# Performance work log

Hardware: AMD Instinct MI355X
Metric: run time of the kernel (lower is better)

Reference implementation:

```python
import jax, jax.numpy as jnp
import numpy as np

NUM_HEADS = 8
FREQ_RATIO = 0.5

def setup_inputs() -> dict:
    key = jax.random.key(0)
    ks = jax.random.split(key, 4)
    B, T, J, C = 16, 256, 17, 512
    x = jax.random.normal(ks[0], (B, T, J, C), jnp.float32)
    w_qkv = jax.random.normal(ks[1], (3 * C, C), jnp.float32) * 0.02
    w_proj = jax.random.normal(ks[2], (C, C), jnp.float32) * 0.02
    b_proj = jnp.zeros((C,), jnp.float32)
    freq_gate = jnp.ones((1,), jnp.float32)
    return {"x": x, "w_qkv": w_qkv, "w_proj": w_proj, "b_proj": b_proj, "freq_gate": freq_gate}

def reference(x, w_qkv, w_proj, b_proj, freq_gate):
    B, T, J, C = x.shape
    H = NUM_HEADS
    hd = C // H
    scale = hd ** (-0.5)
    # qkv projection (no bias): [B,T,J,3,H,hd] -> [3,B,H,T,J,hd]
    qkv = (x @ w_qkv.T).reshape(B, T, J, 3, H, hd)
    qkv = jnp.transpose(qkv, (3, 0, 4, 1, 2, 5))
    q, k, v = qkv[0], qkv[1], qkv[2]
    # temporal layout: [B,H,J,T,hd]
    qt = jnp.swapaxes(q, 2, 3)
    kt = jnp.swapaxes(k, 2, 3)
    vt = jnp.swapaxes(v, 2, 3)
    # ---- time-domain temporal attention ----
    attn = jax.nn.softmax(jnp.einsum('bhjtd,bhjsd->bhjts', qt, kt) * scale, axis=-1)
    x_time = jnp.einsum('bhjts,bhjsd->bhjtd', attn, vt)
    x_time = jnp.transpose(x_time, (0, 3, 2, 1, 4)).reshape(B, T, J, C)
    # ---- frequency-domain temporal attention ----
    qf = jnp.fft.rfft(qt, axis=3)
    kf = jnp.fft.rfft(kt, axis=3)
    vf = jnp.fft.rfft(vt, axis=3)
    f_full = T // 2 + 1
    keep = max(1, int(f_full * FREQ_RATIO))  # low-frequency crop
    qf, kf, vf = qf[:, :, :, :keep], kf[:, :, :, :keep], vf[:, :, :, :keep]
    af = jnp.einsum('bhjfd,bhjgd->bhjfg', qf, jnp.conj(kf)) * scale  # complex [B,H,J,keep,keep]
    af = jax.nn.softmax(af.real, axis=-1) + 1j * jax.nn.softmax(af.imag, axis=-1)
    xf = jnp.einsum('bhjfg,bhjgd->bhjfd', af, vf)
    xf = jnp.pad(xf, ((0, 0), (0, 0), (0, 0), (0, f_full - keep), (0, 0)))  # zero-pad high freqs
    x_freq = jnp.fft.irfft(xf, n=T, axis=3)
    x_freq = jnp.transpose(x_freq, (0, 3, 2, 1, 4)).reshape(B, T, J, C)
    # ---- gated combine + output projection ----
    gate = jax.nn.sigmoid(freq_gate)[0]
    out = gate * x_freq + (1.0 - gate) * x_time
    return out @ w_proj.T + b_proj
```

## Files before the change

### kernel.cpp

```cpp
#include <hip/hip_runtime.h>
#include <hip/hip_fp16.h>
#include <math.h>

#define NB 16
#define TT 256
#define JJ 17
#define CC 512
#define HH 8
#define HD 64
#define MROWS (NB*TT*JJ)
#define QTILE 16384
#define NTILES (NB*HH*JJ)
#define NQKV 35651584

#define FP 68
#define FHALF 4352
#define W0 0.0245436926061702596f

typedef __attribute__((ext_vector_type(8))) short i16x8;
typedef __attribute__((ext_vector_type(8))) _Float16 f16x8;
typedef __attribute__((ext_vector_type(4))) float f32x4;

__device__ __forceinline__ unsigned short f2h(float f) {
    return (unsigned short)__half_as_ushort(__float2half(f));
}
__device__ __forceinline__ float h2f(unsigned short u) {
    return __half2float(__ushort_as_half(u));
}

#define GLD16(gp, lp) __builtin_amdgcn_global_load_lds( \
    (__attribute__((address_space(1))) void*)(gp), \
    (__attribute__((address_space(3))) void*)(lp), 16, 0, 0)

__global__ __launch_bounds__(256) void conv16_k(
    const float* __restrict__ s, unsigned short* __restrict__ d, int n8)
{
    for (int i = blockIdx.x*256 + threadIdx.x; i < n8; i += gridDim.x*256) {
        float4 a = ((const float4*)s)[i*2];
        float4 b = ((const float4*)s)[i*2+1];
        i16x8 h;
        h[0] = (short)f2h(a.x); h[1] = (short)f2h(a.y);
        h[2] = (short)f2h(a.z); h[3] = (short)f2h(a.w);
        h[4] = (short)f2h(b.x); h[5] = (short)f2h(b.y);
        h[6] = (short)f2h(b.z); h[7] = (short)f2h(b.w);
        ((i16x8*)d)[i] = h;
    }
}

__global__ __launch_bounds__(256) void winit_k(
    unsigned short* __restrict__ Whi, unsigned short* __restrict__ Wlo)
{
    const int r = blockIdx.x;
    const int t = threadIdx.x;
    int idx = ((r & 63) * t) & 255;
    float sv, cv;
    sincosf(W0 * (float)idx, &sv, &cv);
    float val = (r < 64) ? cv : -sv;
    unsigned short h = f2h(val);
    Whi[r*256 + t] = h;
    Wlo[r*256 + t] = f2h(val - h2f(h));
}

__global__ __launch_bounds__(128) void winit2_k(unsigned short* __restrict__ WIhi)
{
    const int t = blockIdx.x;
    const int f = threadIdx.x;
    int fr = f & 63;
    int idx = (t * fr) & 255;
    float sv, cv;
    sincosf(W0 * (float)idx, &sv, &cv);
    float cf = (fr == 0 && f < 64) ? 0.5f : 1.f;
    float val = ((f < 64) ? cv : -sv) * cf * (2.f / 256.f);
    WIhi[t*128 + f] = f2h(val);
}

__global__ __launch_bounds__(256) void gemm_qkv_k(
    const unsigned short* __restrict__ A, const unsigned short* __restrict__ B,
    unsigned short* __restrict__ qp, unsigned short* __restrict__ kp,
    unsigned short* __restrict__ vp)
{
    __shared__ unsigned short Ah[128*64];
    __shared__ unsigned short Bh[128*64];
    const int tid = threadIdx.x;
    const int lane = tid & 63;
    const int lo = lane & 15, hi = lane >> 4;
    const int wv = tid >> 6;
    const int wr = wv >> 1, wc = wv & 1;
    const int bid = blockIdx.x;
    const int wrk = (bid & 7) * 816 + (bid >> 3);
    const int col0 = (wrk % 12) * 128;
    const int row0 = (wrk / 12) * 128;

    f32x4 acc[4][4];
    #pragma unroll
    for (int rb = 0; rb < 4; ++rb)
        #pragma unroll
        for (int cb = 0; cb < 4; ++cb) acc[rb][cb] = (f32x4){0.f,0.f,0.f,0.f};

    for (int k0 = 0; k0 < 512; k0 += 64) {
        #pragma unroll
        for (int c = 0; c < 4; ++c) {
            int e = c*2048 + tid*8;
            int r = e >> 6, cc = e & 63;
            int ccs = cc ^ ((r & 7) << 3);
            size_t offA = (size_t)(row0 + r)*512 + k0 + ccs;
            size_t offB = (size_t)(col0 + r)*512 + k0 + ccs;
            GLD16(A + offA, (char*)Ah + c*4096 + tid*16);
            GLD16(B + offB, (char*)Bh + c*4096 + tid*16);
        }
        __syncthreads();
        #pragma unroll
        for (int ks = 0; ks < 2; ++ks) {
            f16x8 af[4], bf[4];
            #pragma unroll
            for (int rb = 0; rb < 4; ++rb) {
                int row = wr*64 + rb*16 + lo;
                int col = (ks*32 + hi*8) ^ ((row & 7) << 3);
                af[rb] = *(const f16x8*)&Ah[row*64 + col];
            }
            #pragma unroll
            for (int cb = 0; cb < 4; ++cb) {
                int row = wc*64 + cb*16 + lo;
                int col = (ks*32 + hi*8) ^ ((row & 7) << 3);
                bf[cb] = *(const f16x8*)&Bh[row*64 + col];
            }
            #pragma unroll
            for (int rb = 0; rb < 4; ++rb)
                #pragma unroll
                for (int cb = 0; cb < 4; ++cb)
                    acc[rb][cb] = __builtin_amdgcn_mfma_f32_16x16x32_f16(
                        af[rb], bf[cb], acc[rb][cb], 0, 0, 0);
        }
        __syncthreads();
    }

    int bbA[4][4], ttA[4][4], jjA[4][4];
    #pragma unroll
    for (int rb = 0; rb < 4; ++rb)
        #pragma unroll
        for (int r = 0; r < 4; ++r) {
            int m = row0 + wr*64 + rb*16 + hi*4 + r;
            int bb = m / (TT*JJ);
            int rem = m - bb*(TT*JJ);
            int t = rem / JJ;
            bbA[rb][r] = bb; ttA[rb][r] = t; jjA[rb][r] = rem - t*JJ;
        }

    #pragma unroll
    for (int cb = 0; cb < 4; ++cb) {
        int n0 = col0 + wc*64 + cb*16;
        int g = n0 >> 9;
        unsigned short* dst0 = (g == 0) ? qp : (g == 1) ? kp : vp;
        float scl = (g == 0) ? 0.125f : 1.f;
        int h = (n0 >> 6) & 7;
        int d = (n0 & 63) + lo;
        #pragma unroll
        for (int rb = 0; rb < 4; ++rb)
            #pragma unroll
            for (int r = 0; r < 4; ++r) {
                size_t off = ((((size_t)bbA[rb][r]*HH + h)*JJ + jjA[rb][r])*TT
                              + ttA[rb][r])*HD + d;
                dst0[off] = f2h(acc[rb][cb][r] * scl);
            }
    }
}

__global__ __launch_bounds__(256) void gemm_proj_k(
    const unsigned short* __restrict__ A, const unsigned short* __restrict__ B,
    const float* __restrict__ bias, float* __restrict__ out)
{
    __shared__ unsigned short Ah[128*64];
    __shared__ unsigned short Bh[128*64];
    const int tid = threadIdx.x;
    const int lane = tid & 63;
    const int lo = lane & 15, hi = lane >> 4;
    const int wv = tid >> 6;
    const int wr = wv >> 1, wc = wv & 1;
    const int bid = blockIdx.x;
    const int wrk = (bid & 7) * 272 + (bid >> 3);
    const int col0 = (wrk % 4) * 128;
    const int row0 = (wrk / 4) * 128;

    f32x4 acc[4][4];
    #pragma unroll
    for (int rb = 0; rb < 4; ++rb)
        #pragma unroll
        for (int cb = 0; cb < 4; ++cb) acc[rb][cb] = (f32x4){0.f,0.f,0.f,0.f};

    for (int k0 = 0; k0 < 512; k0 += 64) {
        #pragma unroll
        for (int c = 0; c < 4; ++c) {
            int e = c*2048 + tid*8;
            int r = e >> 6, cc = e & 63;
            int ccs = cc ^ ((r & 7) << 3);
            size_t offA = (size_t)(row0 + r)*512 + k0 + ccs;
            size_t offB = (size_t)(col0 + r)*512 + k0 + ccs;
            GLD16(A + offA, (char*)Ah + c*4096 + tid*16);
            GLD16(B + offB, (char*)Bh + c*4096 + tid*16);
        }
        __syncthreads();
        #pragma unroll
        for (int ks = 0; ks < 2; ++ks) {
            f16x8 af[4], bf[4];
            #pragma unroll
            for (int rb = 0; rb < 4; ++rb) {
                int row = wr*64 + rb*16 + lo;
                int col = (ks*32 + hi*8) ^ ((row & 7) << 3);
                af[rb] = *(const f16x8*)&Ah[row*64 + col];
            }
            #pragma unroll
            for (int cb = 0; cb < 4; ++cb) {
                int row = wc*64 + cb*16 + lo;
                int col = (ks*32 + hi*8) ^ ((row & 7) << 3);
                bf[cb] = *(const f16x8*)&Bh[row*64 + col];
            }
            #pragma unroll
            for (int rb = 0; rb < 4; ++rb)
                #pragma unroll
                for (int cb = 0; cb < 4; ++cb)
                    acc[rb][cb] = __builtin_amdgcn_mfma_f32_16x16x32_f16(
                        af[rb], bf[cb], acc[rb][cb], 0, 0, 0);
        }
        __syncthreads();
    }

    #pragma unroll
    for (int cb = 0; cb < 4; ++cb) {
        int n = col0 + wc*64 + cb*16 + lo;
        float bv = bias[n];
        #pragma unroll
        for (int rb = 0; rb < 4; ++rb)
            #pragma unroll
            for (int r = 0; r < 4; ++r) {
                int m = row0 + wr*64 + rb*16 + hi*4 + r;
                out[(size_t)m*512 + n] = acc[rb][cb][r] + bv;
            }
    }
}

#define VTP 264
#define PPW 40

__global__ __launch_bounds__(256, 2) void attn_time_k(
    const unsigned short* __restrict__ q, const unsigned short* __restrict__ k,
    const unsigned short* __restrict__ v, const float* __restrict__ fg,
    unsigned short* __restrict__ y)
{
    __shared__ unsigned short VT[64 * VTP];
    __shared__ unsigned short PL[4 * 64 * PPW];

    const int bid = blockIdx.x;
    const int b = bid / (HH*JJ);
    const int h = (bid / JJ) % HH;
    const int j = bid % JJ;
    const size_t base = (size_t)bid * QTILE;

    const int tid = threadIdx.x;
    const int w = tid >> 6;
    const int lane = tid & 63;
    const int lo = lane & 15;
    const int hi = lane >> 4;

    {
        const unsigned short* vptr = v + base + (size_t)tid * HD;
        #pragma unroll
        for (int d0 = 0; d0 < 64; d0 += 8) {
            i16x8 vv = *(const i16x8*)(vptr + d0);
            #pragma unroll
            for (int e = 0; e < 8; ++e)
                VT[(d0+e)*VTP + tid] = (unsigned short)vv[e];
        }
    }
    __syncthreads();

    f16x8 qf[4][2];
    #pragma unroll
    for (int rb = 0; rb < 4; ++rb)
        #pragma unroll
        for (int dc = 0; dc < 2; ++dc)
            qf[rb][dc] = *(const f16x8*)(q + base + (size_t)(w*64 + rb*16 + lo)*HD + dc*32 + hi*8);

    f32x4 o[4][4];
    #pragma unroll
    for (int rb = 0; rb < 4; ++rb)
        #pragma unroll
        for (int cd = 0; cd < 4; ++cd) o[rb][cd] = (f32x4){0.f,0.f,0.f,0.f};
    float rs[4][4];
    #pragma unroll
    for (int rb = 0; rb < 4; ++rb)
        #pragma unroll
        for (int r = 0; r < 4; ++r) rs[rb][r] = 0.f;

    unsigned short* Pw = PL + w * 64 * PPW;

    for (int st = 0; st < 8; ++st) {
        const int s0 = st * 32;
        f16x8 kf[2][2];
        #pragma unroll
        for (int cb = 0; cb < 2; ++cb)
            #pragma unroll
            for (int dc = 0; dc < 2; ++dc)
                kf[cb][dc] = *(const f16x8*)(k + base + (size_t)(s0 + cb*16 + lo)*HD + dc*32 + hi*8);

        #pragma unroll
        for (int rb = 0; rb < 4; ++rb) {
            #pragma unroll
            for (int cb = 0; cb < 2; ++cb) {
                f32x4 acc = (f32x4){0.f,0.f,0.f,0.f};
                acc = __builtin_amdgcn_mfma_f32_16x16x32_f16(qf[rb][0], kf[cb][0], acc, 0, 0, 0);
                acc = __builtin_amdgcn_mfma_f32_16x16x32_f16(qf[rb][1], kf[cb][1], acc, 0, 0, 0);
                #pragma unroll
                for (int r = 0; r < 4; ++r) {
                    float p = __expf(acc[r]);
                    rs[rb][r] += p;
                    Pw[(rb*16 + hi*4 + r)*PPW + cb*16 + lo] = f2h(p);
                }
            }
        }

        f16x8 pa[4];
        #pragma unroll
        for (int rb = 0; rb < 4; ++rb)
            pa[rb] = *(const f16x8*)&Pw[(rb*16 + lo)*PPW + hi*8];
        f16x8 bv[4];
        #pragma unroll
        for (int cd = 0; cd < 4; ++cd)
            bv[cd] = *(const f16x8*)&VT[(cd*16 + lo)*VTP + s0 + hi*8];
        #pragma unroll
        for (int rb = 0; rb < 4; ++rb)
            #pragma unroll
            for (int cd = 0; cd < 4; ++cd)
                o[rb][cd] = __builtin_amdgcn_mfma_f32_16x16x32_f16(pa[rb], bv[cd], o[rb][cd], 0, 0, 0);
    }

    #pragma unroll
    for (int off = 1; off < 16; off <<= 1)
        #pragma unroll
        for (int rb = 0; rb < 4; ++rb)
            #pragma unroll
            for (int r = 0; r < 4; ++r)
                rs[rb][r] += __shfl_xor(rs[rb][r], off, 64);

    const float gate = 1.f / (1.f + __expf(-fg[0]));
    const float wt = 1.f - gate;
    #pragma unroll
    for (int rb = 0; rb < 4; ++rb) {
        #pragma unroll
        for (int r = 0; r < 4; ++r) {
            const int t = w*64 + rb*16 + hi*4 + r;
            const float sc = wt / rs[rb][r];
            unsigned short* yp = y + (((size_t)b*TT + t)*JJ + j)*CC + h*HD;
            #pragma unroll
            for (int cd = 0; cd < 4; ++cd)
                yp[cd*16 + lo] = f2h(o[rb][cd][r] * sc);
        }
    }
}

#define XP 280

__global__ __launch_bounds__(256) void dft_k(
    unsigned short* __restrict__ planes, const unsigned short* __restrict__ Whi,
    const unsigned short* __restrict__ Wlo)
{
    __shared__ unsigned short Xh[64*XP];
    unsigned short* src = planes + (size_t)blockIdx.y*NQKV + (size_t)blockIdx.x*QTILE;
    const int tid = threadIdx.x;
    const int w = tid >> 6;
    const int lane = tid & 63;
    const int qd = (tid >> 4) & 3;
    const int rr = tid & 15;
    const int lo = lane & 15, hi = lane >> 4;

    #pragma unroll
    for (int p = 0; p < 16; ++p) {
        const int t = p*16 + 4*w + qd;
        ushort4 x4 = *(const ushort4*)&src[t*64 + 4*rr];
        unsigned int a0 = x4.x, a1 = x4.y, a2 = x4.z, a3 = x4.w;
        unsigned int t01 = (unsigned)__shfl_xor((int)((qd&1) ? a0 : a1), 16, 64);
        unsigned int t23 = (unsigned)__shfl_xor((int)((qd&1) ? a2 : a3), 16, 64);
        if (qd&1) { a0 = t01; a2 = t23; } else { a1 = t01; a3 = t23; }
        unsigned int u01 = (unsigned)__shfl_xor((int)((qd&2) ? a0 : a2), 32, 64);
        unsigned int u23 = (unsigned)__shfl_xor((int)((qd&2) ? a1 : a3), 32, 64);
        if (qd&2) { a0 = u01; a1 = u23; } else { a2 = u01; a3 = u23; }
        const int dd = 4*rr + qd;
        const int tb = p*16 + 4*w;
        ushort4 hv;
        hv.x = (unsigned short)a0; hv.y = (unsigned short)a1;
        hv.z = (unsigned short)a2; hv.w = (unsigned short)a3;
        *(ushort4*)&Xh[dd*XP + tb] = hv;
    }
    __syncthreads();

    f32x4 acc[2][4];
    #pragma unroll
    for (int rb = 0; rb < 2; ++rb)
        #pragma unroll
        for (int cd = 0; cd < 4; ++cd) acc[rb][cd] = (f32x4){0.f,0.f,0.f,0.f};

    for (int ks = 0; ks < 8; ++ks) {
        const int k0 = ks*32;
        f16x8 ah[2], al[2];
        #pragma unroll
        for (int rb = 0; rb < 2; ++rb) {
            int r = w*32 + rb*16 + lo;
            ah[rb] = *(const f16x8*)&Whi[r*256 + k0 + hi*8];
            al[rb] = *(const f16x8*)&Wlo[r*256 + k0 + hi*8];
        }
        f16x8 bh[4];
        #pragma unroll
        for (int cd = 0; cd < 4; ++cd) {
            int d = cd*16 + lo;
            bh[cd] = *(const f16x8*)&Xh[d*XP + k0 + hi*8];
        }
        #pragma unroll
        for (int rb = 0; rb < 2; ++rb)
            #pragma unroll
            for (int cd = 0; cd < 4; ++cd) {
                acc[rb][cd] = __builtin_amdgcn_mfma_f32_16x16x32_f16(
                    ah[rb], bh[cd], acc[rb][cd], 0, 0, 0);
                acc[rb][cd] = __builtin_amdgcn_mfma_f32_16x16x32_f16(
                    al[rb], bh[cd], acc[rb][cd], 0, 0, 0);
            }
    }

    #pragma unroll
    for (int rb = 0; rb < 2; ++rb) {
        #pragma unroll
        for (int r = 0; r < 4; ++r) {
            int row = w*32 + rb*16 + hi*4 + r;
            unsigned short* dst = (row < 64) ? (src + row*64)
                                             : (src + 4096 + (row-64)*64);
            #pragma unroll
            for (int cd = 0; cd < 4; ++cd)
                dst[cd*16 + lo] = f2h(acc[rb][cd][r]);
        }
    }
}

#define XFP 136

__global__ __launch_bounds__(256) void freqtail_k(
    unsigned short* __restrict__ qfp, const unsigned short* __restrict__ kfp,
    const unsigned short* __restrict__ vfp, const unsigned short* __restrict__ WIhi,
    const float* __restrict__ fg, unsigned short* __restrict__ y)
{
    extern __shared__ float lds[];
    float* A = lds;
    float* B = lds + 2*FHALF;

    const int tid = threadIdx.x;
    const int tile = blockIdx.x;
    const int b = tile / (HH*JJ);
    const int h = (tile / JJ) % HH;
    const int j = tile % JJ;
    const unsigned short* qf = qfp + (size_t)tile * QTILE;
    const unsigned short* kf = kfp + (size_t)tile * QTILE;
    const unsigned short* vf = vfp + (size_t)tile * QTILE;

    #pragma unroll
    for (int p = 0; p < 4; ++p) {
        int idx = p*256 + tid;
        int e8 = idx*8;
        int part = e8 >> 12;
        int row = (e8 >> 6) & 63;
        int col = e8 & 63;
        i16x8 qv = *(const i16x8*)(qf + e8);
        i16x8 kv = *(const i16x8*)(kf + e8);
        float* ap = A + part*FHALF + row*FP + col;
        float* bp = B + part*FHALF + row*FP + col;
        #pragma unroll
        for (int e = 0; e < 8; ++e) {
            ap[e] = h2f((unsigned short)qv[e]);
            bp[e] = h2f((unsigned short)kv[e]);
        }
    }
    __syncthreads();

    const int fy = tid >> 4;
    const int gl = tid & 15;

    float cR[4][4], cI[4][4];
    #pragma unroll
    for (int i = 0; i < 4; ++i)
        #pragma unroll
        for (int gi = 0; gi < 4; ++gi) { cR[i][gi] = 0.f; cI[i][gi] = 0.f; }

    for (int d4 = 0; d4 < 16; ++d4) {
        float4 qr[4], qi[4], kr[4], ki[4];
        #pragma unroll
        for (int i = 0; i < 4; ++i) {
            int f = fy + 16*i;
            qr[i] = *(const float4*)(A + f*FP + d4*4);
            qi[i] = *(const float4*)(A + FHALF + f*FP + d4*4);
            int g = gl + 16*i;
            kr[i] = *(const float4*)(B + g*FP + d4*4);
            ki[i] = *(const float4*)(B + FHALF + g*FP + d4*4);
        }
        #pragma unroll
        for (int i = 0; i < 4; ++i)
            #pragma unroll
            for (int gi = 0; gi < 4; ++gi) {
                float r = cR[i][gi], m = cI[i][gi];
                r = fmaf(qr[i].x, kr[gi].x, r); r = fmaf(qi[i].x, ki[gi].x, r);
                r = fmaf(qr[i].y, kr[gi].y, r); r = fmaf(qi[i].y, ki[gi].y, r);
                r = fmaf(qr[i].z, kr[gi].z, r); r = fmaf(qi[i].z, ki[gi].z, r);
                r = fmaf(qr[i].w, kr[gi].w, r); r = fmaf(qi[i].w, ki[gi].w, r);
                m = fmaf(qi[i].x, kr[gi].x, m); m = fmaf(-qr[i].x, ki[gi].x, m);
                m = fmaf(qi[i].y, kr[gi].y, m); m = fmaf(-qr[i].y, ki[gi].y, m);
                m = fmaf(qi[i].z, kr[gi].z, m); m = fmaf(-qr[i].z, ki[gi].z, m);
                m = fmaf(qi[i].w, kr[gi].w, m); m = fmaf(-qr[i].w, ki[gi].w, m);
                cR[i][gi] = r; cI[i][gi] = m;
            }
    }
    __syncthreads();

    #pragma unroll
    for (int i = 0; i < 4; ++i)
        #pragma unroll
        for (int gi = 0; gi < 4; ++gi) {
            A[(fy + 16*i)*FP + gl + 16*gi]         = cR[i][gi];
            A[FHALF + (fy + 16*i)*FP + gl + 16*gi] = cI[i][gi];
        }
    #pragma unroll
    for (int p = 0; p < 4; ++p) {
        int idx = p*256 + tid;
        int e8 = idx*8;
        int part = e8 >> 12;
        int row = (e8 >> 6) & 63;
        int col = e8 & 63;
        i16x8 vv = *(const i16x8*)(vf + e8);
        float* bp = B + part*FHALF + row*FP + col;
        #pragma unroll
        for (int e = 0; e < 8; ++e) bp[e] = h2f((unsigned short)vv[e]);
    }
    __syncthreads();

    if (tid < 128) {
        float* row = A + (tid >> 6)*FHALF + (tid & 63)*FP;
        float mx = row[0];
        for (int g2 = 1; g2 < 64; ++g2) mx = fmaxf(mx, row[g2]);
        float sum = 0.f;
        for (int g2 = 0; g2 < 64; ++g2) { float e = __expf(row[g2]-mx); row[g2] = e; sum += e; }
        float inv = 1.f / sum;
        for (int g2 = 0; g2 < 64; ++g2) row[g2] *= inv;
    }
    __syncthreads();

    float xR[4][4], xI[4][4];
    #pragma unroll
    for (int i = 0; i < 4; ++i)
        #pragma unroll
        for (int cmp = 0; cmp < 4; ++cmp) { xR[i][cmp] = 0.f; xI[i][cmp] = 0.f; }

    for (int g2 = 0; g2 < 64; ++g2) {
        float4 vr = *(const float4*)(B + g2*FP + gl*4);
        float4 vi = *(const float4*)(B + FHALF + g2*FP + gl*4);
        #pragma unroll
        for (int i = 0; i < 4; ++i) {
            float sr = A[(fy + 16*i)*FP + g2];
            float si = A[FHALF + (fy + 16*i)*FP + g2];
            xR[i][0] = fmaf(sr, vr.x, fmaf(-si, vi.x, xR[i][0]));
            xI[i][0] = fmaf(sr, vi.x, fmaf( si, vr.x, xI[i][0]));
            xR[i][1] = fmaf(sr, vr.y, fmaf(-si, vi.y, xR[i][1]));
            xI[i][1] = fmaf(sr, vi.y, fmaf( si, vr.y, xI[i][1]));
            xR[i][2] = fmaf(sr, vr.z, fmaf(-si, vi.z, xR[i][2]));
            xI[i][2] = fmaf(sr, vi.z, fmaf( si, vr.z, xI[i][2]));
            xR[i][3] = fmaf(sr, vr.w, fmaf(-si, vi.w, xR[i][3]));
            xI[i][3] = fmaf(sr, vi.w, fmaf( si, vr.w, xI[i][3]));
        }
    }
    __syncthreads();

    unsigned short* XT = (unsigned short*)B;
    #pragma unroll
    for (int i = 0; i < 4; ++i) {
        int f = fy + 16*i;
        #pragma unroll
        for (int e = 0; e < 4; ++e) {
            XT[(gl*4+e)*XFP + f]      = f2h(xR[i][e]);
            XT[(gl*4+e)*XFP + 64 + f] = f2h(xI[i][e]);
        }
    }
    __syncthreads();

    const int w = tid >> 6;
    const int lane = tid & 63;
    const int lo = lane & 15, hi = lane >> 4;

    f32x4 acc[4][4];
    #pragma unroll
    for (int rb = 0; rb < 4; ++rb)
        #pragma unroll
        for (int cd = 0; cd < 4; ++cd) acc[rb][cd] = (f32x4){0.f,0.f,0.f,0.f};

    #pragma unroll
    for (int ks = 0; ks < 4; ++ks) {
        const int k0 = ks*32;
        f16x8 ah[4];
        #pragma unroll
        for (int rb = 0; rb < 4; ++rb) {
            int row = w*64 + rb*16 + lo;
            ah[rb] = *(const f16x8*)&WIhi[row*128 + k0 + hi*8];
        }
        f16x8 bt[4];
        #pragma unroll
        for (int cd = 0; cd < 4; ++cd) {
            int d = cd*16 + lo;
            bt[cd] = *(const f16x8*)&XT[d*XFP + k0 + hi*8];
        }
        #pragma unroll
        for (int rb = 0; rb < 4; ++rb)
            #pragma unroll
            for (int cd = 0; cd < 4; ++cd)
                acc[rb][cd] = __builtin_amdgcn_mfma_f32_16x16x32_f16(
                    ah[rb], bt[cd], acc[rb][cd], 0, 0, 0);
    }

    const float gate = 1.f / (1.f + __expf(-fg[0]));
    #pragma unroll
    for (int rb = 0; rb < 4; ++rb) {
        #pragma unroll
        for (int r = 0; r < 4; ++r) {
            int t = w*64 + rb*16 + hi*4 + r;
            unsigned short* yp = y + (((size_t)b*TT + t)*JJ + j)*CC + h*HD;
            #pragma unroll
            for (int cd = 0; cd < 4; ++cd) {
                int d = cd*16 + lo;
                yp[d] = f2h(fmaf(gate, acc[rb][cd][r], h2f(yp[d])));
            }
        }
    }
}

extern "C" void kernel_launch(void* const* d_in, const int* in_sizes, int n_in,
                              void* d_out, int out_size, void* d_ws, size_t ws_size,
                              hipStream_t stream) {
    const float* x      = (const float*)d_in[0];
    const float* w_qkv  = (const float*)d_in[1];
    const float* w_proj = (const float*)d_in[2];
    const float* b_proj = (const float*)d_in[3];
    const float* fg     = (const float*)d_in[4];
    float* out = (float*)d_out;

    unsigned short* qp = (unsigned short*)d_ws;
    unsigned short* kp = qp + NQKV;
    unsigned short* vp = kp + NQKV;
    unsigned short* xh = vp + NQKV;
    unsigned short* y  = xh + NQKV;
    unsigned short* wph = y + NQKV;
    unsigned short* wqh = (unsigned short*)d_out;
    unsigned short* Whi  = wqh + 1536*512;
    unsigned short* Wlo  = Whi + 128*256;
    unsigned short* WIhi = Wlo + 128*256;
    unsigned short* Wend = WIhi + 256*128;
    (void)Wend;

    (void)hipFuncSetAttribute((const void*)freqtail_k,
                              hipFuncAttributeMaxDynamicSharedMemorySize, 4*FHALF*4);

    conv16_k<<<2048, 256, 0, stream>>>(x, xh, NQKV/8);
    conv16_k<<<384, 256, 0, stream>>>(w_qkv, wqh, 1536*512/8);
    conv16_k<<<128, 256, 0, stream>>>(w_proj, wph, 512*512/8);
    winit_k<<<128, 256, 0, stream>>>(Whi, Wlo);
    winit2_k<<<256, 128, 0, stream>>>(WIhi);

    gemm_qkv_k<<<6528, 256, 0, stream>>>(xh, wqh, qp, kp, vp);
    attn_time_k<<<NTILES, 256, 0, stream>>>(qp, kp, vp, fg, y);
    dft_k<<<dim3(NTILES, 3), 256, 0, stream>>>(qp, Whi, Wlo);
    freqtail_k<<<NTILES, 256, 4*FHALF*4, stream>>>(qp, kp, vp, WIhi, fg, y);

    gemm_proj_k<<<2176, 256, 0, stream>>>(y, wph, b_proj, out);
}
```

Baseline: 702.4 us.

## Stage QKV GEMM epilogue through LDS for vectorized scattered stores; merge prep kernels

```diff
diff --git a/kernel.cpp b/kernel.cpp
--- a/kernel.cpp
+++ b/kernel.cpp
@@ -47,31 +47,48 @@
     }
 }
 
-__global__ __launch_bounds__(256) void winit_k(
-    unsigned short* __restrict__ Whi, unsigned short* __restrict__ Wlo)
+__global__ __launch_bounds__(256) void prep_k(
+    const float* __restrict__ wq, const float* __restrict__ wp,
+    unsigned short* __restrict__ wqh, unsigned short* __restrict__ wph,
+    unsigned short* __restrict__ Whi, unsigned short* __restrict__ Wlo,
+    unsigned short* __restrict__ WIhi)
 {
-    const int r = blockIdx.x;
-    const int t = threadIdx.x;
-    int idx = ((r & 63) * t) & 255;
-    float sv, cv;
-    sincosf(W0 * (float)idx, &sv, &cv);
-    float val = (r < 64) ? cv : -sv;
-    unsigned short h = f2h(val);
-    Whi[r*256 + t] = h;
-    Wlo[r*256 + t] = f2h(val - h2f(h));
-}
-
-__global__ __launch_bounds__(128) void winit2_k(unsigned short* __restrict__ WIhi)
-{
-    const int t = blockIdx.x;
-    const int f = threadIdx.x;
-    int fr = f & 63;
-    int idx = (t * fr) & 255;
-    float sv, cv;
-    sincosf(W0 * (float)idx, &sv, &cv);
-    float cf = (fr == 0 && f < 64) ? 0.5f : 1.f;
-    float val = ((f < 64) ? cv : -sv) * cf * (2.f / 256.f);
-    WIhi[t*128 + f] = f2h(val);
+    const int b = blockIdx.x;
+    const int tid = threadIdx.x;
+    if (b < 512) {
+        const float* s = (b < 384) ? wq : wp;
+        unsigned short* d = (b < 384) ? wqh : wph;
+        int i = (b < 384 ? b : b - 384)*256 + tid;
+        float4 a = ((const float4*)s)[i*2];
+        float4 bb = ((const float4*)s)[i*2+1];
+        i16x8 h;
+        h[0] = (short)f2h(a.x); h[1] = (short)f2h(a.y);
+        h[2] = (short)f2h(a.z); h[3] = (short)f2h(a.w);
+        h[4] = (short)f2h(bb.x); h[5] = (short)f2h(bb.y);
+        h[6] = (short)f2h(bb.z); h[7] = (short)f2h(bb.w);
+        ((i16x8*)d)[i] = h;
+    } else if (b < 640) {
+        const int r = b - 512;
+        const int t = tid;
+        int idx = ((r & 63) * t) & 255;
+        float sv, cv;
+        sincosf(W0 * (float)idx, &sv, &cv);
+        float val = (r < 64) ? cv : -sv;
+        unsigned short h = f2h(val);
+        Whi[r*256 + t] = h;
+        Wlo[r*256 + t] = f2h(val - h2f(h));
+    } else {
+        int idx = (b - 640)*256 + tid;
+        int t = idx >> 7;
+        int f = idx & 127;
+        int fr = f & 63;
+        int ii = (t * fr) & 255;
+        float sv, cv;
+        sincosf(W0 * (float)ii, &sv, &cv);
+        float cf = (fr == 0 && f < 64) ? 0.5f : 1.f;
+        float val = ((f < 64) ? cv : -sv) * cf * (2.f / 256.f);
+        WIhi[t*128 + f] = f2h(val);
+    }
 }
 
 __global__ __launch_bounds__(256) void gemm_qkv_k(
@@ -79,8 +96,9 @@
     unsigned short* __restrict__ qp, unsigned short* __restrict__ kp,
     unsigned short* __restrict__ vp)
 {
-    __shared__ unsigned short Ah[128*64];
-    __shared__ unsigned short Bh[128*64];
+    __shared__ unsigned short Sh[128*128];
+    unsigned short* Ah = Sh;
+    unsigned short* Bh = Sh + 128*64;
     const int tid = threadIdx.x;
     const int lane = tid & 63;
     const int lo = lane & 15, hi = lane >> 4;
@@ -134,34 +152,43 @@
         __syncthreads();
     }
 
-    int bbA[4][4], ttA[4][4], jjA[4][4];
-    #pragma unroll
-    for (int rb = 0; rb < 4; ++rb)
-        #pragma unroll
-        for (int r = 0; r < 4; ++r) {
-            int m = row0 + wr*64 + rb*16 + hi*4 + r;
+    #pragma unroll
+    for (int cb = 0; cb < 4; ++cb) {
+        int n0 = col0 + wc*64 + cb*16;
+        float scl = ((n0 >> 9) == 0) ? 0.125f : 1.f;
+        #pragma unroll
+        for (int rb = 0; rb < 4; ++rb)
+            #pragma unroll
+            for (int r = 0; r < 4; ++r) {
+                int row = wr*64 + rb*16 + hi*4 + r;
+                int col = wc*64 + cb*16 + lo;
+                Sh[row*128 + (col ^ ((row & 7) << 3))] = f2h(acc[rb][cb][r]*scl);
+            }
+    }
+    __syncthreads();
+
+    {
+        const int grp = lane >> 3;
+        const int d0 = (lane & 7) * 8;
+        #pragma unroll
+        for (int it = 0; it < 8; ++it) {
+            int p = it*32 + wv*8 + grp;
+            int row = p >> 1;
+            int half = p & 1;
+            int m = row0 + row;
             int bb = m / (TT*JJ);
             int rem = m - bb*(TT*JJ);
             int t = rem / JJ;
-            bbA[rb][r] = bb; ttA[rb][r] = t; jjA[rb][r] = rem - t*JJ;
-        }
-
-    #pragma unroll
-    for (int cb = 0; cb < 4; ++cb) {
-        int n0 = col0 + wc*64 + cb*16;
-        int g = n0 >> 9;
-        unsigned short* dst0 = (g == 0) ? qp : (g == 1) ? kp : vp;
-        float scl = (g == 0) ? 0.125f : 1.f;
-        int h = (n0 >> 6) & 7;
-        int d = (n0 & 63) + lo;
-        #pragma unroll
-        for (int rb = 0; rb < 4; ++rb)
-            #pragma unroll
-            for (int r = 0; r < 4; ++r) {
-                size_t off = ((((size_t)bbA[rb][r]*HH + h)*JJ + jjA[rb][r])*TT
-                              + ttA[rb][r])*HD + d;
-                dst0[off] = f2h(acc[rb][cb][r] * scl);
-            }
+            int j = rem - t*JJ;
+            int n0 = col0 + half*64;
+            int g = n0 >> 9;
+            unsigned short* dst0 = (g == 0) ? qp : (g == 1) ? kp : vp;
+            int h = (n0 >> 6) & 7;
+            unsigned short* dst = dst0 +
+                ((((size_t)bb*HH + h)*JJ + j)*TT + t)*HD + d0;
+            i16x8 vls = *(const i16x8*)&Sh[row*128 + ((half*64 + d0) ^ ((row & 7) << 3))];
+            *(i16x8*)dst = vls;
+        }
     }
 }
 
@@ -653,17 +680,12 @@
     unsigned short* Whi  = wqh + 1536*512;
     unsigned short* Wlo  = Whi + 128*256;
     unsigned short* WIhi = Wlo + 128*256;
-    unsigned short* Wend = WIhi + 256*128;
-    (void)Wend;
 
     (void)hipFuncSetAttribute((const void*)freqtail_k,
                               hipFuncAttributeMaxDynamicSharedMemorySize, 4*FHALF*4);
 
     conv16_k<<<2048, 256, 0, stream>>>(x, xh, NQKV/8);
-    conv16_k<<<384, 256, 0, stream>>>(w_qkv, wqh, 1536*512/8);
-    conv16_k<<<128, 256, 0, stream>>>(w_proj, wph, 512*512/8);
-    winit_k<<<128, 256, 0, stream>>>(Whi, Wlo);
-    winit2_k<<<256, 128, 0, stream>>>(WIhi);
+    prep_k<<<768, 256, 0, stream>>>(w_qkv, w_proj, wqh, wph, Whi, Wlo, WIhi);
 
     gemm_qkv_k<<<6528, 256, 0, stream>>>(xh, wqh, qp, kp, vp);
     attn_time_k<<<NTILES, 256, 0, stream>>>(qp, kp, vp, fg, y);
```

Measured after the change: 688.0 us. 1.02x faster.
